# Kernel tuning notes

Measured on AMD Instinct MI355X. Metric: run time of the kernel, lower is better.

Reference implementation:

```python
import jax, jax.numpy as jnp
import numpy as np

B, S, H, NH = 2, 2048, 2048, 16
HD = H // NH  # 128


def setup_inputs() -> dict:
    key = jax.random.key(0)
    ks = jax.random.split(key, 10)
    scale = 0.02
    hidden_states = jax.random.normal(ks[0], (B, S, H), dtype=jnp.float32)
    # additive causal mask [1,1,S,S]
    causal = jnp.tril(jnp.ones((S, S), dtype=jnp.bool_))
    attention_mask = jnp.where(causal, 0.0, -1e9).astype(jnp.float32)[None, None]
    def lin(k):
        kw, kb = jax.random.split(k)
        return (jax.random.normal(kw, (H, H), dtype=jnp.float32) * scale,
                jnp.zeros((H,), dtype=jnp.float32))
    Wq, bq = lin(ks[1])
    Wk, bk = lin(ks[2])
    Wv, bv = lin(ks[3])
    Wo, bo = lin(ks[4])
    return {"hidden_states": hidden_states, "attention_mask": attention_mask,
            "Wq": Wq, "bq": bq, "Wk": Wk, "bk": bk, "Wv": Wv, "bv": bv,
            "Wo": Wo, "bo": bo}


def reference(hidden_states, attention_mask, Wq, bq, Wk, bk, Wv, bv, Wo, bo):
    b, s, h = hidden_states.shape
    def shape(t):  # [b,s,h] -> [b,nh,s,hd]
        return t.reshape(b, s, NH, HD).transpose(0, 2, 1, 3)
    q = shape(hidden_states @ Wq.T + bq)
    k = shape(hidden_states @ Wk.T + bk)
    v = shape(hidden_states @ Wv.T + bv)
    attn = jnp.einsum('bnqd,bnkd->bnqk', q, k) / jnp.sqrt(jnp.float32(HD))
    attn = attn + attention_mask
    attn = jax.nn.softmax(attn, axis=-1)
    out = jnp.einsum('bnqk,bnkd->bnqd', attn, v)
    out = out.transpose(0, 2, 1, 3).reshape(b, s, h)
    return out @ Wo.T + bo
```

## Files before the change

kernel.cpp:

```cpp
#include <hip/hip_runtime.h>
#include <hip/hip_bf16.h>

#define SEQ   2048
#define HDIM  2048
#define NHEAD 16
#define HEADD 128
#define BATCH 2
#define MTOT  (BATCH*SEQ)
#define BH    (BATCH*NHEAD)

typedef __attribute__((ext_vector_type(8))) __bf16 bf16x8;
typedef __attribute__((ext_vector_type(4))) float f32x4;
typedef __attribute__((ext_vector_type(16))) float f32x16;
typedef __attribute__((ext_vector_type(8))) unsigned short u16x8;

__device__ __forceinline__ unsigned short f2b(float f) {
    __bf16 h = (__bf16)f;
    return __builtin_bit_cast(unsigned short, h);
}

__device__ __forceinline__ void gld_lds16(const void* gptr, void* ldsptr) {
    __builtin_amdgcn_global_load_lds(
        (const __attribute__((address_space(1))) unsigned int*)gptr,
        (__attribute__((address_space(3))) unsigned int*)ldsptr,
        16, 0, 0);
}

__global__ void cvt_bf16(const float* __restrict__ src, unsigned short* __restrict__ dst, long n8) {
    long i = blockIdx.x * (long)blockDim.x + threadIdx.x;
    long stride = (long)gridDim.x * blockDim.x;
    for (; i < n8; i += stride) {
        f32x4 a = *(const f32x4*)(src + i * 8);
        f32x4 b = *(const f32x4*)(src + i * 8 + 4);
        u16x8 o;
#pragma unroll
        for (int j = 0; j < 4; ++j) { o[j] = f2b(a[j]); o[4 + j] = f2b(b[j]); }
        *(u16x8*)(dst + i * 8) = o;
    }
}

__global__ void cvt5(const float* __restrict__ s0, const float* __restrict__ s1,
                     const float* __restrict__ s2, const float* __restrict__ s3,
                     const float* __restrict__ s4,
                     unsigned short* __restrict__ d0, unsigned short* __restrict__ d1,
                     unsigned short* __restrict__ d2, unsigned short* __restrict__ d3,
                     unsigned short* __restrict__ d4,
                     long n0, long n1) {
    const float* s; unsigned short* d; long n;
    switch (blockIdx.z) {
        case 0: s = s0; d = d0; n = n0; break;
        case 1: s = s1; d = d1; n = n1; break;
        case 2: s = s2; d = d2; n = n1; break;
        case 3: s = s3; d = d3; n = n1; break;
        default: s = s4; d = d4; n = n1; break;
    }
    long i = blockIdx.x * (long)blockDim.x + threadIdx.x;
    long stride = (long)gridDim.x * blockDim.x;
    for (; i < n; i += stride) {
        f32x4 a = *(const f32x4*)(s + i * 8);
        f32x4 b = *(const f32x4*)(s + i * 8 + 4);
        u16x8 o;
#pragma unroll
        for (int j = 0; j < 4; ++j) { o[j] = f2b(a[j]); o[4 + j] = f2b(b[j]); }
        *(u16x8*)(d + i * 8) = o;
    }
}

template <int MODE>
__launch_bounds__(256)
__global__ void gemm_bt(const unsigned short* __restrict__ A,
                        const unsigned short* __restrict__ Bw,
                        const float* __restrict__ bias,
                        void* __restrict__ Cout,
                        int Kc, float scale) {
    __shared__ unsigned short As[128 * 32];
    __shared__ unsigned short Bs[128 * 32];
    const int tid  = threadIdx.x;
    const int lane = tid & 63;
    const int w    = tid >> 6;

    const int wgid = blockIdx.y * gridDim.x + blockIdx.x;
    const int cpx  = (gridDim.x * gridDim.y) >> 3;
    const int swz  = (wgid & 7) * cpx + (wgid >> 3);
    const int m0 = (swz % gridDim.x) * 128, n0 = (swz / gridDim.x) * 128;

    const int wr = (w >> 1) * 64, wc = (w & 1) * 64;
    const long rowBytes = (long)Kc * 2;

    f32x4 acc[4][4] = {};

    const int kIters = Kc >> 5;
    for (int kt = 0; kt < kIters; ++kt) {
        const long kb = (long)kt * 64;
#pragma unroll
        for (int i = 0; i < 2; ++i) {
            int c = tid + i * 256;
            int row = c >> 2;
            int cb  = (c & 3) * 16;
            gld_lds16((const char*)A  + (long)(m0 + row) * rowBytes + kb + cb, (char*)As + c * 16);
            gld_lds16((const char*)Bw + (long)(n0 + row) * rowBytes + kb + cb, (char*)Bs + c * 16);
        }
        __syncthreads();
        bf16x8 af[4], bfr[4];
#pragma unroll
        for (int f = 0; f < 4; ++f) {
            af[f]  = *(const bf16x8*)&As[(wr + f * 16 + (lane & 15)) * 32 + (lane >> 4) * 8];
            bfr[f] = *(const bf16x8*)&Bs[(wc + f * 16 + (lane & 15)) * 32 + (lane >> 4) * 8];
        }
#pragma unroll
        for (int mf = 0; mf < 4; ++mf)
#pragma unroll
            for (int nf = 0; nf < 4; ++nf)
                acc[mf][nf] = __builtin_amdgcn_mfma_f32_16x16x32_bf16(af[mf], bfr[nf], acc[mf][nf], 0, 0, 0);
        __syncthreads();
    }

#pragma unroll
    for (int mf = 0; mf < 4; ++mf) {
#pragma unroll
        for (int nf = 0; nf < 4; ++nf) {
            int n = n0 + wc + nf * 16 + (lane & 15);
            float bv = bias[n];
#pragma unroll
            for (int j = 0; j < 4; ++j) {
                int m = m0 + wr + mf * 16 + (lane >> 4) * 4 + j;
                float v = (acc[mf][nf][j] + bv) * scale;
                if (MODE == 0) {
                    int b = m >> 11, s = m & 2047;
                    int nh = n >> 7, hd = n & 127;
                    ((unsigned short*)Cout)[((long)(b * NHEAD + nh) * SEQ + s) * HEADD + hd] = f2b(v);
                } else if (MODE == 1) {
                    int b = m >> 11, s = m & 2047;
                    int nh = n >> 7, hd = n & 127;
                    ((unsigned short*)Cout)[((long)(b * NHEAD + nh) * HEADD + hd) * SEQ + s] = f2b(v);
                } else {
                    ((float*)Cout)[(long)m * HDIM + n] = v;
                }
            }
        }
    }
}


#define MASKV (-3.0e38f)

__device__ __forceinline__ void attn_step32s(
    const unsigned short* Ksb, const unsigned short* Vsb,
    const bf16x8 (&qf)[8], f32x16 (&acc)[4], float& mrun, float& lrun,
    int lane, int p, int q0w, int kvt, bool diag)
{
    const int ql = lane & 31;
    const int hi = lane >> 5;

    f32x16 sv = {};
    {
        const int row = p * 32 + ql;
        const int sw  = (row & 7) << 4;
        __builtin_amdgcn_s_setprio(1);
#pragma unroll
        for (int kc = 0; kc < 8; ++kc) {
            int off = (row * 256 + ((kc * 32 + hi * 16) ^ sw)) >> 1;
            bf16x8 kf = *(const bf16x8*)&Ksb[off];
            sv = __builtin_amdgcn_mfma_f32_32x32x16_bf16(kf, qf[kc], sv, 0, 0, 0);
        }
        __builtin_amdgcn_s_setprio(0);
    }

    if (diag) {
        const int qg = q0w + ql;
#pragma unroll
        for (int r = 0; r < 16; ++r) {
            int kv = kvt * 64 + p * 32 + (r & 3) + 8 * (r >> 2) + 4 * hi;
            if (kv > qg) sv[r] = MASKV;
        }
    }

    float tmax = sv[0];
#pragma unroll
    for (int r = 1; r < 16; ++r) tmax = fmaxf(tmax, sv[r]);
    tmax = fmaxf(tmax, __shfl_xor(tmax, 32));

    float mnew = mrun, sc = 1.0f;
    if (__any(tmax > mrun + 8.0f)) {
        mnew = fmaxf(mrun, tmax);
        sc = __expf(mrun - mnew);
#pragma unroll
        for (int db = 0; db < 4; ++db) acc[db] *= sc;
    }
    float rsum = 0.f;
#pragma unroll
    for (int r = 0; r < 16; ++r) {
        float pv = __expf(sv[r] - mnew);
        sv[r] = pv;
        rsum += pv;
    }
    rsum += __shfl_xor(rsum, 32);
    lrun = lrun * sc + rsum;
    mrun = mnew;

    bf16x8 pf[2];
#pragma unroll
    for (int kc2 = 0; kc2 < 2; ++kc2) {
        unsigned int w01 = f2b(sv[8 * kc2 + 0]) | ((unsigned int)f2b(sv[8 * kc2 + 1]) << 16);
        unsigned int w23 = f2b(sv[8 * kc2 + 2]) | ((unsigned int)f2b(sv[8 * kc2 + 3]) << 16);
        unsigned int w45 = f2b(sv[8 * kc2 + 4]) | ((unsigned int)f2b(sv[8 * kc2 + 5]) << 16);
        unsigned int w67 = f2b(sv[8 * kc2 + 6]) | ((unsigned int)f2b(sv[8 * kc2 + 7]) << 16);
        asm volatile("v_permlane32_swap_b32 %0, %1" : "+v"(w01), "+v"(w45));
        asm volatile("v_permlane32_swap_b32 %0, %1" : "+v"(w23), "+v"(w67));
        union { unsigned int u[4]; bf16x8 v; } pk;
        pk.u[0] = w01; pk.u[1] = w23; pk.u[2] = w45; pk.u[3] = w67;
        pf[kc2] = pk.v;
    }

    __builtin_amdgcn_s_setprio(1);
#pragma unroll
    for (int db = 0; db < 4; ++db) {
        const int row = db * 32 + ql;
        const int sw  = (row & 7) << 4;
#pragma unroll
        for (int kc2 = 0; kc2 < 2; ++kc2) {
            int off = (row * 128 + ((p * 64 + kc2 * 32 + hi * 16) ^ sw)) >> 1;
            bf16x8 vf = *(const bf16x8*)&Vsb[off];
            acc[db] = __builtin_amdgcn_mfma_f32_32x32x16_bf16(vf, pf[kc2], acc[db], 0, 0, 0);
        }
    }
    __builtin_amdgcn_s_setprio(0);
}

__device__ __forceinline__ void attn_merge_store(
    f32x16 (&acc)[4], float mrun, float lrun,
    float (*Mx)[32], float (*Lx)[32], f32x16 (*Ob)[64],
    unsigned short* __restrict__ Out, long rowbase, int lane, int wp, int p)
{
    const int ql = lane & 31, hi = lane >> 5;
    Mx[wp * 2 + p][ql] = mrun;
    Lx[wp * 2 + p][ql] = lrun;
    __syncthreads();
    const float mo = Mx[wp * 2 + 1 - p][ql];
    const float lo = Lx[wp * 2 + 1 - p][ql];
    const float M  = fmaxf(mrun, mo);
    const float a  = __expf(mrun - M);
    const float L  = lrun * a + lo * __expf(mo - M);
#pragma unroll
    for (int db = 0; db < 4; ++db) acc[db] *= a;
#pragma unroll
    for (int db = 0; db < 4; ++db) {
        if (p == 1) Ob[wp][lane] = acc[db];
        __syncthreads();
        if (p == 0) acc[db] += Ob[wp][lane];
        __syncthreads();
    }
    if (p == 0) {
        const float inv = 1.0f / L;
        const long base = rowbase + (long)ql * HDIM;
#pragma unroll
        for (int db = 0; db < 4; ++db)
#pragma unroll
            for (int mm = 0; mm < 4; ++mm) {
                int d0 = db * 32 + 8 * mm + 4 * hi;
                unsigned int w0 = f2b(acc[db][4 * mm + 0] * inv) | ((unsigned int)f2b(acc[db][4 * mm + 1] * inv) << 16);
                unsigned int w1 = f2b(acc[db][4 * mm + 2] * inv) | ((unsigned int)f2b(acc[db][4 * mm + 3] * inv) << 16);
                *(unsigned long long*)(Out + base + d0) =
                    (unsigned long long)w0 | ((unsigned long long)w1 << 32);
            }
    }
}

__launch_bounds__(512, 1)
__global__ void attn_fwd(const unsigned short* __restrict__ Q,
                         const unsigned short* __restrict__ K,
                         const unsigned short* __restrict__ Vt,
                         unsigned short* __restrict__ Out) {
    __shared__ unsigned short Ks[2][64 * 128];
    __shared__ unsigned short Vs[2][128 * 64];
    __shared__ float Mx[8][32];
    __shared__ float Lx[8][32];
    __shared__ f32x16 Ob[4][64];

    const int tid  = threadIdx.x;
    const int lane = tid & 63;
    const int w    = tid >> 6;
    const int wp   = w & 3;
    const int p    = w >> 2;

    const int id  = blockIdx.x;
    const int xcd = id & 7;
    const int j   = id >> 3;
    const int bh  = xcd * 4 + (j >> 3);
    const int x   = j & 7;
    const int hiT = 15 - x;
    const int loT = x;
    const int nA  = 2 * hiT + 2;
    const int nB  = 2 * loT + 2;
    const int q0A = hiT * 128 + wp * 32;
    const int q0B = loT * 128 + wp * 32;

    const char* Kbase = (const char*)(K  + (long)bh * SEQ * HEADD);
    const char* Vbase = (const char*)(Vt + (long)bh * HEADD * SEQ);

#define STAGE(kvt, bb) do {                                                             \
    _Pragma("unroll")                                                                   \
    for (int i = 0; i < 2; ++i) {                                                       \
        int c = tid + i * 512;                                                          \
        int rowk = c >> 4;                                                              \
        int cbk  = ((c & 15) * 16) ^ ((rowk & 7) << 4);                                 \
        gld_lds16(Kbase + (long)((kvt) * 64 + rowk) * 256 + cbk, (char*)Ks[bb] + c * 16);\
        int rowv = c >> 3;                                                              \
        int cbv  = ((c & 7) * 16) ^ ((rowv & 7) << 4);                                  \
        gld_lds16(Vbase + (long)rowv * (SEQ * 2) + (kvt) * 128 + cbv, (char*)Vs[bb] + c * 16); \
    } } while (0)

    const int b = bh >> 4, nh = bh & 15;
    int buf = 0;

    STAGE(0, 0);
    __syncthreads();

    {
        bf16x8 qf[8];
#pragma unroll
        for (int kc = 0; kc < 8; ++kc)
            qf[kc] = *(const bf16x8*)&Q[((long)bh * SEQ + q0A + (lane & 31)) * HEADD + kc * 16 + (lane >> 5) * 8];

        f32x16 acc[4] = {};
        float mrun = -1e30f, lrun = 0.f;
        for (int s = 0; s < nA; ++s) {
            if (s + 1 < nA) STAGE(s + 1, buf ^ 1);
            else            STAGE(0, buf ^ 1);
            attn_step32s(Ks[buf], Vs[buf], qf, acc, mrun, lrun,
                         lane, p, q0A, s, s * 64 + 63 > q0A);
            __syncthreads();
            buf ^= 1;
        }
        attn_merge_store(acc, mrun, lrun, Mx, Lx, Ob, Out,
                         ((long)(b * SEQ) + q0A) * HDIM + nh * HEADD, lane, wp, p);
    }

    {
        bf16x8 qf[8];
#pragma unroll
        for (int kc = 0; kc < 8; ++kc)
            qf[kc] = *(const bf16x8*)&Q[((long)bh * SEQ + q0B + (lane & 31)) * HEADD + kc * 16 + (lane >> 5) * 8];

        f32x16 acc[4] = {};
        float mrun = -1e30f, lrun = 0.f;
        for (int s = 0; s < nB; ++s) {
            if (s + 1 < nB) STAGE(s + 1, buf ^ 1);
            attn_step32s(Ks[buf], Vs[buf], qf, acc, mrun, lrun,
                         lane, p, q0B, s, s * 64 + 63 > q0B);
            __syncthreads();
            buf ^= 1;
        }
        attn_merge_store(acc, mrun, lrun, Mx, Lx, Ob, Out,
                         ((long)(b * SEQ) + q0B) * HDIM + nh * HEADD, lane, wp, p);
    }
#undef STAGE
}

extern "C" void kernel_launch(void* const* d_in, const int* in_sizes, int n_in,
                              void* d_out, int out_size, void* d_ws, size_t ws_size,
                              hipStream_t stream) {
    const float* hs = (const float*)d_in[0];
    const float* Wq = (const float*)d_in[2];
    const float* bq = (const float*)d_in[3];
    const float* Wk = (const float*)d_in[4];
    const float* bk = (const float*)d_in[5];
    const float* Wv = (const float*)d_in[6];
    const float* bv = (const float*)d_in[7];
    const float* Wo = (const float*)d_in[8];
    const float* bo = (const float*)d_in[9];
    float* out = (float*)d_out;

    char* ws = (char*)d_ws;
    const long MB = 1024L * 1024L;
    const float rs = 0.08838834764831845f;
    dim3 gg(MTOT / 128, HDIM / 128);

    if (ws_size >= 96 * MB) {
        unsigned short* hsb  = (unsigned short*)ws;
        unsigned short* wqkv = (unsigned short*)(ws + 16 * MB);
        unsigned short* wob  = (unsigned short*)(ws + 40 * MB);
        unsigned short* qb   = (unsigned short*)(ws + 48 * MB);
        unsigned short* kb   = (unsigned short*)(ws + 64 * MB);
        unsigned short* vtb  = (unsigned short*)(ws + 80 * MB);
        unsigned short* aob  = hsb;
        unsigned short* wqb  = wqkv;
        unsigned short* wkb  = wqkv + 2048L * 2048;
        unsigned short* wvb  = wqkv + 2L * 2048 * 2048;

        cvt5<<<dim3(1024, 1, 5), 256, 0, stream>>>(
            hs, Wq, Wk, Wv, Wo,
            hsb, wqb, wkb, wvb, wob,
            (long)MTOT * HDIM / 8, (long)HDIM * HDIM / 8);
        gemm_bt<0><<<gg, 256, 0, stream>>>(hsb, wqb, bq, qb,  HDIM, rs);
        gemm_bt<0><<<gg, 256, 0, stream>>>(hsb, wkb, bk, kb,  HDIM, 1.0f);
        gemm_bt<1><<<gg, 256, 0, stream>>>(hsb, wvb, bv, vtb, HDIM, 1.0f);
        attn_fwd<<<256, 512, 0, stream>>>(qb, kb, vtb, aob);
        gemm_bt<2><<<gg, 256, 0, stream>>>(aob, wob, bo, out, HDIM, 1.0f);
    } else {
        unsigned short* hsb = (unsigned short*)ws;
        unsigned short* wb  = (unsigned short*)(ws + 16 * MB);
        unsigned short* qb  = (unsigned short*)(ws + 24 * MB);
        unsigned short* kb  = (unsigned short*)(ws + 40 * MB);
        unsigned short* vtb = (unsigned short*)(ws + 56 * MB);
        unsigned short* aob = hsb;

        cvt_bf16<<<2048, 256, 0, stream>>>(hs, hsb, (long)MTOT * HDIM / 8);
        cvt_bf16<<<2048, 256, 0, stream>>>(Wq, wb, (long)HDIM * HDIM / 8);
        gemm_bt<0><<<gg, 256, 0, stream>>>(hsb, wb, bq, qb, HDIM, rs);
        cvt_bf16<<<2048, 256, 0, stream>>>(Wk, wb, (long)HDIM * HDIM / 8);
        gemm_bt<0><<<gg, 256, 0, stream>>>(hsb, wb, bk, kb, HDIM, 1.0f);
        cvt_bf16<<<2048, 256, 0, stream>>>(Wv, wb, (long)HDIM * HDIM / 8);
        gemm_bt<1><<<gg, 256, 0, stream>>>(hsb, wb, bv, vtb, HDIM, 1.0f);
        attn_fwd<<<256, 512, 0, stream>>>(qb, kb, vtb, aob);
        cvt_bf16<<<2048, 256, 0, stream>>>(Wo, wb, (long)HDIM * HDIM / 8);
        gemm_bt<2><<<gg, 256, 0, stream>>>(aob, wb, bo, out, HDIM, 1.0f);
    }
}
```

Baseline: 311.0 us.

## Fuse Q/K/V projections into one GEMM launch and switch softmax to exp2

Replaces three separate projection GEMM launches with a single kernel over a concatenated QKV weight (grid 32x48). Each block picks its bias, scale and output layout (head-major for Q/K, transposed for V) from its column range. The softmax now uses exp2f with log2(e) folded into the Q scale, and the lazy rescale threshold is widened to match base-2 units. The output GEMM gets its own specialised kernel without the scale multiply. The aims are fewer launches with a fuller grid per wave, and cheaper exponentials in attention.

```diff
diff --git a/kernel.cpp b/kernel.cpp
--- a/kernel.cpp
+++ b/kernel.cpp
@@ -66,13 +66,12 @@
     }
 }
 
-template <int MODE>
 __launch_bounds__(256)
-__global__ void gemm_bt(const unsigned short* __restrict__ A,
-                        const unsigned short* __restrict__ Bw,
-                        const float* __restrict__ bias,
-                        void* __restrict__ Cout,
-                        int Kc, float scale) {
+__global__ void gemm_qkv(const unsigned short* __restrict__ A,
+                         const unsigned short* __restrict__ Bw,
+                         const float* __restrict__ bq, const float* __restrict__ bk,
+                         const float* __restrict__ bv,
+                         unsigned short* __restrict__ Cout, float rs) {
     __shared__ unsigned short As[128 * 32];
     __shared__ unsigned short Bs[128 * 32];
     const int tid  = threadIdx.x;
@@ -82,14 +81,91 @@
     const int wgid = blockIdx.y * gridDim.x + blockIdx.x;
     const int cpx  = (gridDim.x * gridDim.y) >> 3;
     const int swz  = (wgid & 7) * cpx + (wgid >> 3);
+    const int m0  = (swz % gridDim.x) * 128;
+    const int n0g = (swz / gridDim.x) * 128;
+
+    const int wr = (w >> 1) * 64, wc = (w & 1) * 64;
+    const long rowBytes = (long)HDIM * 2;
+
+    const char* Ab = (const char*)A  + (long)m0  * rowBytes;
+    const char* Bb = (const char*)Bw + (long)n0g * rowBytes;
+
+    f32x4 acc[4][4] = {};
+
+    const int kIters = HDIM >> 5;
+    for (int kt = 0; kt < kIters; ++kt) {
+        const long kb = (long)kt * 64;
+#pragma unroll
+        for (int i = 0; i < 2; ++i) {
+            int c = tid + i * 256;
+            int row = c >> 2;
+            int cb  = (c & 3) * 16;
+            gld_lds16(Ab + (long)row * rowBytes + kb + cb, (char*)As + c * 16);
+            gld_lds16(Bb + (long)row * rowBytes + kb + cb, (char*)Bs + c * 16);
+        }
+        __syncthreads();
+        bf16x8 af[4], bfr[4];
+#pragma unroll
+        for (int f = 0; f < 4; ++f) {
+            af[f]  = *(const bf16x8*)&As[(wr + f * 16 + (lane & 15)) * 32 + (lane >> 4) * 8];
+            bfr[f] = *(const bf16x8*)&Bs[(wc + f * 16 + (lane & 15)) * 32 + (lane >> 4) * 8];
+        }
+#pragma unroll
+        for (int mf = 0; mf < 4; ++mf)
+#pragma unroll
+            for (int nf = 0; nf < 4; ++nf)
+                acc[mf][nf] = __builtin_amdgcn_mfma_f32_16x16x32_bf16(af[mf], bfr[nf], acc[mf][nf], 0, 0, 0);
+        __syncthreads();
+    }
+
+    const int mat = n0g >> 11;
+    const float* bb = (mat == 0) ? bq : (mat == 1) ? bk : bv;
+    const float scale = (mat == 0) ? rs : 1.0f;
+    unsigned short* O = Cout + (long)mat * 8388608;
+
+#pragma unroll
+    for (int mf = 0; mf < 4; ++mf) {
+#pragma unroll
+        for (int nf = 0; nf < 4; ++nf) {
+            int nn = (n0g + wc + nf * 16 + (lane & 15)) & 2047;
+            int nh = nn >> 7, hd = nn & 127;
+            float bv_ = bb[nn];
+#pragma unroll
+            for (int j = 0; j < 4; ++j) {
+                int m = m0 + wr + mf * 16 + (lane >> 4) * 4 + j;
+                int b = m >> 11, s = m & 2047;
+                float v = (acc[mf][nf][j] + bv_) * scale;
+                long idx;
+                if (mat < 2) idx = ((long)(b * NHEAD + nh) * SEQ + s) * HEADD + hd;
+                else         idx = ((long)(b * NHEAD + nh) * HEADD + hd) * SEQ + s;
+                O[idx] = f2b(v);
+            }
+        }
+    }
+}
+
+__launch_bounds__(256)
+__global__ void gemm_out(const unsigned short* __restrict__ A,
+                         const unsigned short* __restrict__ Bw,
+                         const float* __restrict__ bias,
+                         float* __restrict__ Cout) {
+    __shared__ unsigned short As[128 * 32];
+    __shared__ unsigned short Bs[128 * 32];
+    const int tid  = threadIdx.x;
+    const int lane = tid & 63;
+    const int w    = tid >> 6;
+
+    const int wgid = blockIdx.y * gridDim.x + blockIdx.x;
+    const int cpx  = (gridDim.x * gridDim.y) >> 3;
+    const int swz  = (wgid & 7) * cpx + (wgid >> 3);
     const int m0 = (swz % gridDim.x) * 128, n0 = (swz / gridDim.x) * 128;
 
     const int wr = (w >> 1) * 64, wc = (w & 1) * 64;
-    const long rowBytes = (long)Kc * 2;
+    const long rowBytes = (long)HDIM * 2;
 
     f32x4 acc[4][4] = {};
 
-    const int kIters = Kc >> 5;
+    const int kIters = HDIM >> 5;
     for (int kt = 0; kt < kIters; ++kt) {
         const long kb = (long)kt * 64;
 #pragma unroll
@@ -124,23 +200,11 @@
 #pragma unroll
             for (int j = 0; j < 4; ++j) {
                 int m = m0 + wr + mf * 16 + (lane >> 4) * 4 + j;
-                float v = (acc[mf][nf][j] + bv) * scale;
-                if (MODE == 0) {
-                    int b = m >> 11, s = m & 2047;
-                    int nh = n >> 7, hd = n & 127;
-                    ((unsigned short*)Cout)[((long)(b * NHEAD + nh) * SEQ + s) * HEADD + hd] = f2b(v);
-                } else if (MODE == 1) {
-                    int b = m >> 11, s = m & 2047;
-                    int nh = n >> 7, hd = n & 127;
-                    ((unsigned short*)Cout)[((long)(b * NHEAD + nh) * HEADD + hd) * SEQ + s] = f2b(v);
-                } else {
-                    ((float*)Cout)[(long)m * HDIM + n] = v;
-                }
+                Cout[(long)m * HDIM + n] = acc[mf][nf][j] + bv;
             }
         }
     }
 }
-
 
 #define MASKV (-3.0e38f)
 
@@ -181,16 +245,16 @@
     tmax = fmaxf(tmax, __shfl_xor(tmax, 32));
 
     float mnew = mrun, sc = 1.0f;
-    if (__any(tmax > mrun + 8.0f)) {
+    if (__any(tmax > mrun + 11.5f)) {
         mnew = fmaxf(mrun, tmax);
-        sc = __expf(mrun - mnew);
+        sc = exp2f(mrun - mnew);
 #pragma unroll
         for (int db = 0; db < 4; ++db) acc[db] *= sc;
     }
     float rsum = 0.f;
 #pragma unroll
     for (int r = 0; r < 16; ++r) {
-        float pv = __expf(sv[r] - mnew);
+        float pv = exp2f(sv[r] - mnew);
         sv[r] = pv;
         rsum += pv;
     }
@@ -239,8 +303,8 @@
     const float mo = Mx[wp * 2 + 1 - p][ql];
     const float lo = Lx[wp * 2 + 1 - p][ql];
     const float M  = fmaxf(mrun, mo);
-    const float a  = __expf(mrun - M);
-    const float L  = lrun * a + lo * __expf(mo - M);
+    const float a  = exp2f(mrun - M);
+    const float L  = lrun * a + lo * exp2f(mo - M);
 #pragma unroll
     for (int db = 0; db < 4; ++db) acc[db] *= a;
 #pragma unroll
@@ -373,8 +437,7 @@
 
     char* ws = (char*)d_ws;
     const long MB = 1024L * 1024L;
-    const float rs = 0.08838834764831845f;
-    dim3 gg(MTOT / 128, HDIM / 128);
+    const float rs = 0.08838834764831845f * 1.4426950408889634f;
 
     if (ws_size >= 96 * MB) {
         unsigned short* hsb  = (unsigned short*)ws;
@@ -392,28 +455,24 @@
             hs, Wq, Wk, Wv, Wo,
             hsb, wqb, wkb, wvb, wob,
             (long)MTOT * HDIM / 8, (long)HDIM * HDIM / 8);
-        gemm_bt<0><<<gg, 256, 0, stream>>>(hsb, wqb, bq, qb,  HDIM, rs);
-        gemm_bt<0><<<gg, 256, 0, stream>>>(hsb, wkb, bk, kb,  HDIM, 1.0f);
-        gemm_bt<1><<<gg, 256, 0, stream>>>(hsb, wvb, bv, vtb, HDIM, 1.0f);
+        gemm_qkv<<<dim3(32, 48), 256, 0, stream>>>(hsb, wqkv, bq, bk, bv, qb, rs);
         attn_fwd<<<256, 512, 0, stream>>>(qb, kb, vtb, aob);
-        gemm_bt<2><<<gg, 256, 0, stream>>>(aob, wob, bo, out, HDIM, 1.0f);
+        gemm_out<<<dim3(32, 16), 256, 0, stream>>>(aob, wob, bo, out);
     } else {
         unsigned short* hsb = (unsigned short*)ws;
         unsigned short* wb  = (unsigned short*)(ws + 16 * MB);
-        unsigned short* qb  = (unsigned short*)(ws + 24 * MB);
-        unsigned short* kb  = (unsigned short*)(ws + 40 * MB);
-        unsigned short* vtb = (unsigned short*)(ws + 56 * MB);
+        unsigned short* qb  = (unsigned short*)(ws + 40 * MB);
+        unsigned short* kb  = (unsigned short*)(ws + 56 * MB);
+        unsigned short* vtb = (unsigned short*)(ws + 72 * MB);
         unsigned short* aob = hsb;
 
         cvt_bf16<<<2048, 256, 0, stream>>>(hs, hsb, (long)MTOT * HDIM / 8);
         cvt_bf16<<<2048, 256, 0, stream>>>(Wq, wb, (long)HDIM * HDIM / 8);
-        gemm_bt<0><<<gg, 256, 0, stream>>>(hsb, wb, bq, qb, HDIM, rs);
-        cvt_bf16<<<2048, 256, 0, stream>>>(Wk, wb, (long)HDIM * HDIM / 8);
-        gemm_bt<0><<<gg, 256, 0, stream>>>(hsb, wb, bk, kb, HDIM, 1.0f);
-        cvt_bf16<<<2048, 256, 0, stream>>>(Wv, wb, (long)HDIM * HDIM / 8);
-        gemm_bt<1><<<gg, 256, 0, stream>>>(hsb, wb, bv, vtb, HDIM, 1.0f);
+        cvt_bf16<<<2048, 256, 0, stream>>>(Wk, wb + 2048L * 2048, (long)HDIM * HDIM / 8);
+        cvt_bf16<<<2048, 256, 0, stream>>>(Wv, wb + 2L * 2048 * 2048, (long)HDIM * HDIM / 8);
+        gemm_qkv<<<dim3(32, 48), 256, 0, stream>>>(hsb, wb, bq, bk, bv, qb, rs);
         attn_fwd<<<256, 512, 0, stream>>>(qb, kb, vtb, aob);
         cvt_bf16<<<2048, 256, 0, stream>>>(Wo, wb, (long)HDIM * HDIM / 8);
-        gemm_bt<2><<<gg, 256, 0, stream>>>(aob, wb, bo, out, HDIM, 1.0f);
-    }
-}
+        gemm_out<<<dim3(32, 16), 256, 0, stream>>>(aob, wb == 0 ? (const unsigned short*)0 : wb, bo, out);
+    }
+}
```

Result: faster. 295.8 us (-4.9%).
